# Kernel optimization log

Hardware: AMD Instinct MI355X
Metric: run time of the kernel (lower is better)

The kernel has to match this reference:

```python
import jax, jax.numpy as jnp
import numpy as np

WS = 16          # window_size
OWS = 24         # overlap_win_size = int(ws*0.5) + ws
PAD = (OWS - WS) // 2
NH = 6           # num_heads


def _ln(x, g, b):
    m = jnp.mean(x, axis=-1, keepdims=True)
    v = jnp.mean((x - m) ** 2, axis=-1, keepdims=True)
    return (x - m) * jax.lax.rsqrt(v + 1e-5) * g + b


def setup_inputs() -> dict:
    key = jax.random.key(0)
    ks = jax.random.split(key, 12)
    B, H, W, C = 4, 64, 64, 180
    std = 0.02
    x = jax.random.normal(ks[0], (B, H * W, C), jnp.float32)
    y = jax.random.normal(ks[1], (B, H * W, C), jnp.float32)
    kv_w = jax.random.normal(ks[2], (2 * C, C), jnp.float32) * std
    kv_b = jnp.zeros((2 * C,), jnp.float32)
    q_w = jax.random.normal(ks[3], (C, C), jnp.float32) * std
    q_b = jnp.zeros((C,), jnp.float32)
    rpb = jax.random.normal(ks[4], ((WS + OWS - 1) ** 2, NH), jnp.float32) * std
    proj_w = jax.random.normal(ks[5], (C, C), jnp.float32) * std
    proj_b = jnp.zeros((C,), jnp.float32)
    fc1_w = jax.random.normal(ks[6], (4 * C, C), jnp.float32) * std
    fc1_b = jnp.zeros((4 * C,), jnp.float32)
    fc2_w = jax.random.normal(ks[7], (C, 4 * C), jnp.float32) * std
    fc2_b = jnp.zeros((C,), jnp.float32)
    norm1_g = jnp.ones((C,), jnp.float32); norm1_b = jnp.zeros((C,), jnp.float32)
    norm2_g = jnp.ones((C,), jnp.float32); norm2_b = jnp.zeros((C,), jnp.float32)
    # relative position index (HAT-style OCA): query coords vs extended window coords
    co = np.stack(np.meshgrid(np.arange(WS), np.arange(WS), indexing='ij')).reshape(2, -1)   # 2, ws*ws
    ce = np.stack(np.meshgrid(np.arange(OWS), np.arange(OWS), indexing='ij')).reshape(2, -1) # 2, ows*ows
    rel = (ce[:, None, :] - co[:, :, None]).transpose(1, 2, 0) + (WS - 1)  # nq, n, 2 in [0, ws+ows-2]
    rpi = jnp.asarray(rel[..., 0] * (WS + OWS - 1) + rel[..., 1], jnp.int32)  # [256, 576]
    return {
        'x': x, 'y': y,
        'norm1_g': norm1_g, 'norm1_b': norm1_b,
        'kv_w': kv_w, 'kv_b': kv_b, 'q_w': q_w, 'q_b': q_b,
        'rpb': rpb, 'proj_w': proj_w, 'proj_b': proj_b,
        'norm2_g': norm2_g, 'norm2_b': norm2_b,
        'fc1_w': fc1_w, 'fc1_b': fc1_b, 'fc2_w': fc2_w, 'fc2_b': fc2_b,
        'rpi': rpi, 'h': 64, 'w': 64,
    }


def reference(x, y, norm1_g, norm1_b, kv_w, kv_b, q_w, q_b, rpb, proj_w, proj_b,
              norm2_g, norm2_b, fc1_w, fc1_b, fc2_w, fc2_b, rpi, h, w):
    b, L, c = x.shape
    nh = NH
    d = c // nh
    scale = d ** -0.5
    nwh, nww = h // WS, w // WS
    nq, n = WS * WS, OWS * OWS

    shortcut = x
    xn = _ln(x, norm1_g, norm1_b).reshape(b, h, w, c)
    yn = _ln(y, norm1_g, norm1_b).reshape(b, h, w, c)

    kv = xn @ kv_w.T + kv_b                                  # b,h,w,2c
    q = yn @ q_w.T + q_b                                     # b,h,w,c

    # kv -> [2, b, c, h, w] then pad spatially and extract overlapping windows (nn.Unfold)
    kv = kv.reshape(b, h, w, 2, c).transpose(3, 0, 4, 1, 2)  # 2,b,c,h,w
    kvp = jnp.pad(kv, ((0, 0), (0, 0), (0, 0), (PAD, PAD), (PAD, PAD)))
    hh = jnp.arange(nwh)[:, None] * WS + jnp.arange(OWS)[None, :]   # [nwh, OWS]
    ww = jnp.arange(nww)[:, None] * WS + jnp.arange(OWS)[None, :]   # [nww, OWS]
    patches = kvp[:, :, :, hh][:, :, :, :, :, ww]            # 2,b,c,nwh,OWS,nww,OWS
    kvw = patches.transpose(0, 1, 3, 5, 4, 6, 2).reshape(2, b * nwh * nww, n, c)
    kwin, vwin = kvw[0], kvw[1]                              # [b_, n, c]

    # non-overlapping query windows (window_partition)
    qwin = q.reshape(b, nwh, WS, nww, WS, c).transpose(0, 1, 3, 2, 4, 5).reshape(-1, nq, c)
    b_ = qwin.shape[0]

    qh = qwin.reshape(b_, nq, nh, d).transpose(0, 2, 1, 3) * scale
    kh = kwin.reshape(b_, n, nh, d).transpose(0, 2, 1, 3)
    vh = vwin.reshape(b_, n, nh, d).transpose(0, 2, 1, 3)

    attn = jnp.einsum('bhqd,bhkd->bhqk', qh, kh)             # [b_, nh, nq, n]
    bias = rpb[rpi.reshape(-1)].reshape(nq, n, nh).transpose(2, 0, 1)  # [nh, nq, n]
    attn = jax.nn.softmax(attn + bias[None], axis=-1)
    out = jnp.einsum('bhqk,bhkd->bhqd', attn, vh).transpose(0, 2, 1, 3).reshape(b_, nq, c)

    # window_reverse
    out = out.reshape(b, nwh, nww, WS, WS, c).transpose(0, 1, 3, 2, 4, 5).reshape(b, h * w, c)

    xo = out @ proj_w.T + proj_b + shortcut
    xn2 = _ln(xo, norm2_g, norm2_b)
    mlp = jax.nn.gelu(xn2 @ fc1_w.T + fc1_b, approximate=False) @ fc2_w.T + fc2_b
    return xo + mlp
```

## Files before the change

kernel.cpp:

```cpp
#include <hip/hip_runtime.h>

typedef __bf16 bf16;
typedef __bf16 bf16x8 __attribute__((ext_vector_type(8)));
typedef __bf16 bf16x4 __attribute__((ext_vector_type(4)));
typedef __bf16 bf16x2 __attribute__((ext_vector_type(2)));
typedef float f32x4 __attribute__((ext_vector_type(4)));

static __device__ __forceinline__ bf16x8 ld8(const bf16* p) {
    return *reinterpret_cast<const bf16x8*>(p);
}
static __device__ __forceinline__ bf16x4 ld4(const bf16* p) {
    return *reinterpret_cast<const bf16x4*>(p);
}
static __device__ __forceinline__ bf16x8 ld8_b32(const bf16* p) {
    bf16x8 v;
#pragma unroll
    for (int i = 0; i < 4; ++i) {
        bf16x2 t = *reinterpret_cast<const bf16x2*>(p + i * 2);
        v[i * 2] = t[0]; v[i * 2 + 1] = t[1];
    }
    return v;
}
static __device__ __forceinline__ bf16x8 zero8() {
    bf16x8 v;
#pragma unroll
    for (int i = 0; i < 8; ++i) v[i] = (bf16)0.f;
    return v;
}

#define MFMA16(a, b, c) __builtin_amdgcn_mfma_f32_16x16x32_bf16((a), (b), (c), 0, 0, 0)

template <int ROWS, int BK, int KPAD, int THREADS>
static __device__ __forceinline__ void load_chunk_g(const bf16* __restrict__ g,
                                                    bf16x8* r, int tid) {
    constexpr int TOT = ROWS * BK / 8;
    constexpr int NP = (TOT + THREADS - 1) / THREADS;
#pragma unroll
    for (int p = 0; p < NP; ++p) {
        int idx = p * THREADS + tid;
        if ((TOT % THREADS) == 0 || idx < TOT) {
            int row = idx / (BK / 8), cg = idx % (BK / 8);
            r[p] = ld8(g + (long)row * KPAD + cg * 8);
        }
    }
}
template <int ROWS, int BK, int THREADS>
static __device__ __forceinline__ void store_chunk_l(bf16* __restrict__ lds,
                                                     const bf16x8* r, int tid) {
    constexpr int TOT = ROWS * BK / 8;
    constexpr int NP = (TOT + THREADS - 1) / THREADS;
#pragma unroll
    for (int p = 0; p < NP; ++p) {
        int idx = p * THREADS + tid;
        if ((TOT % THREADS) == 0 || idx < TOT) {
            int row = idx / (BK / 8), cg = idx % (BK / 8);
            *reinterpret_cast<bf16x8*>(lds + row * 200 + cg * 8) = r[p];
        }
    }
}
template <int ROWS, int BK, int KPAD, int THREADS>
static __device__ __forceinline__ void stage_tile(const bf16* __restrict__ g,
                                                  bf16* __restrict__ lds, int tid) {
    constexpr int TOT = ROWS * BK / 8;
    constexpr int NP = (TOT + THREADS - 1) / THREADS;
#pragma unroll
    for (int p = 0; p < NP; ++p) {
        int idx = p * THREADS + tid;
        if ((TOT % THREADS) == 0 || idx < TOT) {
            int row = idx / (BK / 8), cg = idx % (BK / 8);
            bf16x8 v = ld8(g + (long)row * KPAD + cg * 8);
            *reinterpret_cast<bf16x8*>(lds + row * 200 + cg * 8) = v;
        }
    }
}

__global__ __launch_bounds__(256) void fused_pre(
    const float* __restrict__ x, const float* __restrict__ y,
    const float* __restrict__ g, const float* __restrict__ b,
    bf16* __restrict__ dst,
    const float* __restrict__ kv_w, const float* __restrict__ kv_b,
    const float* __restrict__ q_w, const float* __restrict__ q_b,
    const float* __restrict__ proj_w, const float* __restrict__ fc1_w,
    const float* __restrict__ fc2_w, const float* __restrict__ rpb,
    const int* __restrict__ rpi,
    bf16* __restrict__ wkv, bf16* __restrict__ wq, bf16* __restrict__ wproj,
    bf16* __restrict__ wfc1, bf16* __restrict__ wfc2, bf16* __restrict__ biast,
    float* __restrict__ kvbp, float* __restrict__ qbp)
{
    for (int u = blockIdx.x; u < 13635; u += 1704) {
        if (u < 8192) {
            int wave = threadIdx.x >> 6, lane = threadIdx.x & 63;
            int row = u * 4 + wave;
            const float* sp = (row < 16384) ? (x + (long)row * 180)
                                            : (y + (long)(row - 16384) * 180);
            float v0 = sp[lane];
            float v1 = sp[lane + 64];
            float v2 = (lane < 52) ? sp[lane + 128] : 0.f;
            float s = v0 + v1 + v2;
            float sq = v0 * v0 + v1 * v1 + v2 * v2;
#pragma unroll
            for (int m = 32; m >= 1; m >>= 1) {
                s += __shfl_xor(s, m);
                sq += __shfl_xor(sq, m);
            }
            float mean = s * (1.f / 180.f);
            float var = sq * (1.f / 180.f) - mean * mean;
            float rs = rsqrtf(var + 1e-5f);
            bf16* dp = dst + (long)row * 192;
            dp[lane] = (bf16)((v0 - mean) * rs * g[lane] + b[lane]);
            dp[lane + 64] = (bf16)((v1 - mean) * rs * g[lane + 64] + b[lane + 64]);
            float o2 = (lane < 52) ? ((v2 - mean) * rs * g[lane + 128] + b[lane + 128]) : 0.f;
            dp[lane + 128] = (bf16)o2;
            continue;
        }
        int i = (u - 8192) * 256 + threadIdx.x;
        if (i < 73728) {
            int n = i / 192, k = i % 192;
            int kv = n / 192, rem = n % 192, hh = rem >> 5, d = rem & 31;
            float v = (d < 30 && k < 180) ? kv_w[(kv * 180 + hh * 30 + d) * 180 + k] : 0.f;
            wkv[i] = (bf16)v;
        } else if (i < 122880) {
            int j = i - 73728; int n = j / 192, k = j % 192;
            int hh = n >> 5, d = n & 31;
            float v = (n < 192 && d < 30 && k < 180) ? q_w[(hh * 30 + d) * 180 + k] : 0.f;
            wq[j] = (bf16)v;
        } else if (i < 172032) {
            int j = i - 122880; int n = j / 192, k = j % 192;
            int hh = k >> 5, d = k & 31;
            float v = (n < 180 && d < 30) ? proj_w[n * 180 + hh * 30 + d] : 0.f;
            wproj[j] = (bf16)v;
        } else if (i < 319488) {
            int j = i - 172032; int n = j / 192, k = j % 192;
            float v = (n < 720 && k < 180) ? fc1_w[n * 180 + k] : 0.f;
            wfc1[j] = (bf16)v;
        } else if (i < 507904) {
            int j = i - 319488; int n = j / 736, k = j % 736;
            float v = (n < 180 && k < 720) ? fc2_w[n * 720 + k] : 0.f;
            wfc2[j] = (bf16)v;
        } else if (i < 1392640) {
            int t = i - 507904;
            int r = t & 3;
            int lane = (t >> 2) & 63;
            int tmp2 = t >> 8;
            int kg = tmp2 % 36;
            int tmp3 = tmp2 / 36;
            int qg = tmp3 & 15;
            int h = tmp3 >> 4;
            int q = qg * 16 + (lane & 15);
            int key = kg * 16 + ((lane >> 4) << 2) + r;
            biast[t] = (bf16)rpb[rpi[q * 576 + key] * 6 + h];
        } else if (i < 1393024) {
            int t = i - 1392640;
            int kv = t / 192, rem = t % 192, hh = rem >> 5, d = rem & 31;
            kvbp[t] = (d < 30) ? kv_b[kv * 180 + hh * 30 + d] : 0.f;
        } else if (i < 1393216) {
            int t = i - 1393024;
            int hh = t >> 5, d = t & 31;
            qbp[t] = (d < 30) ? q_b[hh * 30 + d] * 0.18257418583505537f : 0.f;
        }
    }
}

__global__ __launch_bounds__(256, 3) void gemm_kvq(
    const bf16* __restrict__ xn, const bf16* __restrict__ yn,
    const bf16* __restrict__ wkv, const bf16* __restrict__ wq,
    const float* __restrict__ kvbp, const float* __restrict__ qbp,
    bf16* __restrict__ kvbuf, bf16* __restrict__ qbuf)
{
    const int tid = threadIdx.x, wave = tid >> 6, lane = tid & 63;
    const int llo = lane & 15, quad = lane >> 4;
    const int phys = blockIdx.x;
    const int xcd = phys & 7, idx = phys >> 3;
    const int tmi = xcd * 32 + idx / 3;
    const int bz = idx % 3;
    const bool isq = (bz == 2);
    const bf16* A = isq ? yn : xn;
    const bf16* Wbase = isq ? wq : (wkv + (long)bz * 3 * 64 * 192);
    const int tm = tmi * 64;

    __shared__ __align__(16) bf16 Sa[64 * 200];
    __shared__ __align__(16) bf16 Sb[64 * 200];
    bf16* Sc = Sb;

    stage_tile<64, 192, 192, 256>(A + (long)tm * 192, Sa, tid);
    bf16x8 wreg[6];
    load_chunk_g<64, 192, 192, 256>(Wbase, wreg, tid);

    const float sc = isq ? 0.18257418583505537f : 1.f;

    for (int s = 0; s < 3; ++s) {
        if (s) __syncthreads();
        store_chunk_l<64, 192, 256>(Sb, wreg, tid);
        __syncthreads();
        if (s < 2) load_chunk_g<64, 192, 192, 256>(Wbase + (long)(s + 1) * 64 * 192, wreg, tid);

        f32x4 acc[4];
#pragma unroll
        for (int nt = 0; nt < 4; ++nt)
#pragma unroll
            for (int r = 0; r < 4; ++r) acc[nt][r] = 0.f;
#pragma unroll
        for (int kt = 0; kt < 6; ++kt) {
            bf16x8 a = ld8(Sa + (wave * 16 + llo) * 200 + kt * 32 + quad * 8);
#pragma unroll
            for (int nt = 0; nt < 4; ++nt) {
                bf16x8 b = ld8(Sb + (nt * 16 + llo) * 200 + kt * 32 + quad * 8);
                acc[nt] = MFMA16(a, b, acc[nt]);
            }
        }

        const int grp = bz * 3 + s;
        __syncthreads();
#pragma unroll
        for (int nt = 0; nt < 4; ++nt) {
            int n = grp * 64 + nt * 16 + llo;
            float bv = isq ? qbp[n - 384] : kvbp[n];
#pragma unroll
            for (int r = 0; r < 4; ++r)
                Sc[(wave * 16 + quad * 4 + r) * 72 + nt * 16 + llo] =
                    (bf16)(acc[nt][r] * sc + bv);
        }
        __syncthreads();
#pragma unroll
        for (int ps = 0; ps < 2; ++ps) {
            int un = ps * 256 + tid;
            int row = un >> 3, seg = un & 7;
            bf16x8 vv = *reinterpret_cast<const bf16x8*>(Sc + row * 72 + seg * 8);
            long m = tm + row;
            if (!isq)
                *reinterpret_cast<bf16x8*>(kvbuf + m * 384 + grp * 64 + seg * 8) = vv;
            else
                *reinterpret_cast<bf16x8*>(qbuf + m * 192 + (grp - 6) * 64 + seg * 8) = vv;
        }
    }
}

__global__ __launch_bounds__(512, 6) void attn_kernel(
    const bf16* __restrict__ qbuf, const bf16* __restrict__ kvbuf,
    const bf16* __restrict__ biast, bf16* __restrict__ obuf)
{
    const int phys = blockIdx.x;
    const int xcd = phys & 7, idx = phys >> 3;
    const int win = xcd * 8 + idx / 12;
    const int sub = idx % 12;
    const int qhalf = sub & 1;
    const int head = sub >> 1;
    const int bb = win / 16, wi = (win % 16) / 4, wj = win % 4;
    const int tid = threadIdx.x;
    const int wave = tid >> 6, lane = tid & 63;
    const int llo = lane & 15, quad = lane >> 4;
    const int qbase = qhalf * 128 + wave * 16;
    const int qg = qhalf * 8 + wave;

    __shared__ bf16 Kc[2][64][40];
    __shared__ bf16 Vt[2][32][74];
    __shared__ bf16 Ps[8][16][72];

    const int u = tid & 255;
    const int tloc = u >> 2, dq = u & 3;
    const bool isV = tid >= 256;
    int aa = tloc / 24, w0 = tloc % 24;

    const int q0 = qbase + llo;
    const int gr_q = bb * 4096 + (wi * 16 + (q0 >> 4)) * 64 + (wj * 16 + (q0 & 15));
    const bf16x8 qf = ld8(qbuf + (long)gr_q * 192 + head * 32 + quad * 8);
    const bf16* bbase = biast + ((long)(head * 16 + qg) * 36) * 256 + lane * 4;

    {
        int gy = wi * 16 + aa - 4, gx = wj * 16 + w0 - 4;
        bf16x8 st = zero8();
        if ((unsigned)gy < 64u && (unsigned)gx < 64u) {
            long gr = (long)(bb * 4096 + gy * 64 + gx) * 384;
            st = ld8(kvbuf + gr + (isV ? 192 : 0) + head * 32 + dq * 8);
        }
        if (!isV) {
            *reinterpret_cast<bf16x8*>(&Kc[0][tloc][dq * 8]) = st;
        } else {
#pragma unroll
            for (int j = 0; j < 8; ++j) Vt[0][dq * 8 + j][tloc] = st[j];
        }
    }
    __syncthreads();

    f32x4 o[2];
    float m_run = -1e30f, l_run = 0.f;
#pragma unroll
    for (int n2 = 0; n2 < 2; ++n2)
#pragma unroll
        for (int r = 0; r < 4; ++r) o[n2][r] = 0.f;

    for (int c = 0; c < 9; ++c) {
        const int cur = c & 1;

        bf16x8 stage;
        if (c < 8) {
            w0 += 16; aa += 2;
            if (w0 >= 24) { w0 -= 24; ++aa; }
            int gy = wi * 16 + aa - 4, gx = wj * 16 + w0 - 4;
            stage = zero8();
            if ((unsigned)gy < 64u && (unsigned)gx < 64u) {
                long gr = (long)(bb * 4096 + gy * 64 + gx) * 384;
                stage = ld8(kvbuf + gr + (isV ? 192 : 0) + head * 32 + dq * 8);
            }
        }

        f32x4 s[4];
#pragma unroll
        for (int kt = 0; kt < 4; ++kt) {
            bf16x8 kf = ld8(&Kc[cur][kt * 16 + llo][quad * 8]);
            f32x4 zc;
            zc[0] = 0.f; zc[1] = 0.f; zc[2] = 0.f; zc[3] = 0.f;
            s[kt] = MFMA16(kf, qf, zc);
        }

#pragma unroll
        for (int kt = 0; kt < 4; ++kt) {
            bf16x4 bv = ld4(bbase + (c * 4 + kt) * 256);
#pragma unroll
            for (int r = 0; r < 4; ++r) s[kt][r] += (float)bv[r];
        }

        float mx = s[0][0];
#pragma unroll
        for (int kt = 0; kt < 4; ++kt)
#pragma unroll
            for (int r = 0; r < 4; ++r) mx = fmaxf(mx, s[kt][r]);
        mx = fmaxf(mx, __shfl_xor(mx, 16));
        mx = fmaxf(mx, __shfl_xor(mx, 32));
        float m_new = fmaxf(m_run, mx);
        float alpha = __expf(m_run - m_new);
        float ls = 0.f;
#pragma unroll
        for (int kt = 0; kt < 4; ++kt)
#pragma unroll
            for (int r = 0; r < 4; ++r) {
                float p = __expf(s[kt][r] - m_new);
                s[kt][r] = p;
                ls += p;
            }
        ls += __shfl_xor(ls, 16);
        ls += __shfl_xor(ls, 32);
        l_run = l_run * alpha + ls;
        m_run = m_new;

#pragma unroll
        for (int r = 0; r < 4; ++r) {
            float a = __shfl(alpha, quad * 4 + r);
            o[0][r] *= a;
            o[1][r] *= a;
        }

#pragma unroll
        for (int kt = 0; kt < 4; ++kt) {
            bf16x4 pv;
#pragma unroll
            for (int r = 0; r < 4; ++r) pv[r] = (bf16)s[kt][r];
            *reinterpret_cast<bf16x4*>(&Ps[wave][llo][kt * 16 + quad * 4]) = pv;
        }

#pragma unroll
        for (int kt2 = 0; kt2 < 2; ++kt2) {
            bf16x8 pa = ld8(&Ps[wave][llo][kt2 * 32 + quad * 8]);
#pragma unroll
            for (int n2 = 0; n2 < 2; ++n2) {
                bf16x8 vb = ld8_b32(&Vt[cur][n2 * 16 + llo][kt2 * 32 + quad * 8]);
                o[n2] = MFMA16(pa, vb, o[n2]);
            }
        }

        if (c < 8) {
            if (!isV) {
                *reinterpret_cast<bf16x8*>(&Kc[1 - cur][tloc][dq * 8]) = stage;
            } else {
#pragma unroll
                for (int j = 0; j < 8; ++j) Vt[1 - cur][dq * 8 + j][tloc] = stage[j];
            }
            __syncthreads();
        }
    }

    float linv = 1.f / l_run;
#pragma unroll
    for (int r = 0; r < 4; ++r) {
        float li = __shfl(linv, quad * 4 + r);
        int q = qbase + quad * 4 + r;
        int gr = bb * 4096 + (wi * 16 + (q >> 4)) * 64 + (wj * 16 + (q & 15));
#pragma unroll
        for (int n2 = 0; n2 < 2; ++n2)
            obuf[(long)gr * 192 + head * 32 + n2 * 16 + llo] = (bf16)(o[n2][r] * li);
    }
}

__global__ __launch_bounds__(256, 3) void gemm_projln(
    const bf16* __restrict__ obuf, const bf16* __restrict__ wproj,
    const float* __restrict__ proj_b, const float* __restrict__ x,
    const float* __restrict__ g, const float* __restrict__ bln,
    float* __restrict__ xo, bf16* __restrict__ xn2)
{
    const int tid = threadIdx.x, wave = tid >> 6, lane = tid & 63;
    const int llo = lane & 15, quad = lane >> 4;
    const int mbase = blockIdx.x * 64;

    __shared__ __align__(16) bf16 Sa[64 * 200];
    __shared__ __align__(16) bf16 Sb[64 * 200];
    stage_tile<64, 192, 192, 256>(obuf + (long)mbase * 192, Sa, tid);
    bf16x8 wreg[6];
    load_chunk_g<64, 192, 192, 256>(wproj, wreg, tid);

    f32x4 acc[12];
#pragma unroll
    for (int nt = 0; nt < 12; ++nt)
#pragma unroll
        for (int r = 0; r < 4; ++r) acc[nt][r] = 0.f;

    for (int nc = 0; nc < 3; ++nc) {
        if (nc) __syncthreads();
        store_chunk_l<64, 192, 256>(Sb, wreg, tid);
        __syncthreads();
        if (nc < 2) load_chunk_g<64, 192, 192, 256>(wproj + (long)(nc + 1) * 64 * 192, wreg, tid);
#pragma unroll
        for (int kt = 0; kt < 6; ++kt) {
            bf16x8 a = ld8(Sa + (wave * 16 + llo) * 200 + kt * 32 + quad * 8);
#pragma unroll
            for (int nt = 0; nt < 4; ++nt) {
                bf16x8 b = ld8(Sb + (nt * 16 + llo) * 200 + kt * 32 + quad * 8);
                acc[nc * 4 + nt] = MFMA16(a, b, acc[nc * 4 + nt]);
            }
        }
    }

#pragma unroll
    for (int r = 0; r < 4; ++r) {
        int m = mbase + wave * 16 + quad * 4 + r;
        float v[12];
        float sum = 0.f, sq = 0.f;
#pragma unroll
        for (int nt = 0; nt < 12; ++nt) {
            int n = nt * 16 + llo;
            float val = 0.f;
            if (n < 180) val = acc[nt][r] + proj_b[n] + x[(long)m * 180 + n];
            v[nt] = val;
            sum += val; sq += val * val;
        }
#pragma unroll
        for (int msk = 1; msk <= 8; msk <<= 1) {
            sum += __shfl_xor(sum, msk);
            sq  += __shfl_xor(sq, msk);
        }
        float mean = sum * (1.f / 180.f);
        float var = sq * (1.f / 180.f) - mean * mean;
        float rs = rsqrtf(var + 1e-5f);
#pragma unroll
        for (int nt = 0; nt < 12; ++nt) {
            int n = nt * 16 + llo;
            if (n < 180) {
                xo[(long)m * 180 + n] = v[nt];
                xn2[(long)m * 192 + n] = (bf16)((v[nt] - mean) * rs * g[n] + bln[n]);
            } else {
                xn2[(long)m * 192 + n] = (bf16)0.f;
            }
        }
    }
}

__global__ __launch_bounds__(512, 4) void gemm_fc1(
    const bf16* __restrict__ A, const bf16* __restrict__ W,
    const float* __restrict__ bias, bf16* __restrict__ outp)
{
    const int tid = threadIdx.x, wave = tid >> 6, lane = tid & 63;
    const int llo = lane & 15, quad = lane >> 4;
    const int phys = blockIdx.x;
    const int xcd = phys & 7, idx = phys >> 3;
    const int tmi = xcd * 16 + idx / 4;
    const int bz = idx % 4;
    const int tm = tmi * 128;
    const bf16* Wbase = W + (long)bz * 3 * 64 * 192;

    __shared__ __align__(16) bf16 Sa[128 * 200];
    __shared__ __align__(16) bf16 Sb[64 * 200];
    bf16* Sc = Sb;

    stage_tile<128, 192, 192, 512>(A + (long)tm * 192, Sa, tid);
    bf16x8 wreg[3];
    load_chunk_g<64, 192, 192, 512>(Wbase, wreg, tid);

    for (int s = 0; s < 3; ++s) {
        if (s) __syncthreads();
        store_chunk_l<64, 192, 512>(Sb, wreg, tid);
        __syncthreads();
        if (s < 2) load_chunk_g<64, 192, 192, 512>(Wbase + (long)(s + 1) * 64 * 192, wreg, tid);

        f32x4 acc[4];
#pragma unroll
        for (int nt = 0; nt < 4; ++nt)
#pragma unroll
            for (int r = 0; r < 4; ++r) acc[nt][r] = 0.f;
#pragma unroll
        for (int kt = 0; kt < 6; ++kt) {
            bf16x8 a = ld8(Sa + (wave * 16 + llo) * 200 + kt * 32 + quad * 8);
#pragma unroll
            for (int nt = 0; nt < 4; ++nt) {
                bf16x8 b = ld8(Sb + (nt * 16 + llo) * 200 + kt * 32 + quad * 8);
                acc[nt] = MFMA16(a, b, acc[nt]);
            }
        }

        const int nb = (bz * 3 + s) * 64;
        __syncthreads();
#pragma unroll
        for (int nt = 0; nt < 4; ++nt) {
            int n = nb + nt * 16 + llo;
            float bv = (n < 720) ? bias[n] : 0.f;
#pragma unroll
            for (int r = 0; r < 4; ++r) {
                float v = acc[nt][r] + bv;
                float gel = 0.5f * v * (1.f + erff(v * 0.7071067811865475f));
                Sc[(wave * 16 + quad * 4 + r) * 72 + nt * 16 + llo] = (bf16)gel;
            }
        }
        __syncthreads();
        const int row8 = tid >> 3, seg = tid & 7;
        if (nb + seg * 8 < 736) {
#pragma unroll
            for (int ps = 0; ps < 2; ++ps) {
                int row = ps * 64 + row8;
                bf16x8 vv = *reinterpret_cast<const bf16x8*>(Sc + row * 72 + seg * 8);
                *reinterpret_cast<bf16x8*>(outp + (long)(tm + row) * 736 + nb + seg * 8) = vv;
            }
        }
    }
}

__global__ __launch_bounds__(256, 4) void gemm_fc2(
    const bf16* __restrict__ A, const bf16* __restrict__ W,
    const float* __restrict__ bias, const float* __restrict__ resid,
    float* __restrict__ outp)
{
    const int tid = threadIdx.x, wave = tid >> 6, lane = tid & 63;
    const int llo = lane & 15, quad = lane >> 4;
    const int phys = blockIdx.x;
    const int xcd = phys & 7, idx = phys >> 3;
    const int tmi = xcd * 32 + idx / 3;
    const int tni = idx % 3;
    const int tm = tmi * 64;
    const int tn = tni * 64;

    __shared__ __align__(16) bf16 Sa[64 * 200];
    __shared__ __align__(16) bf16 Sb[64 * 200];

    const bf16* Ap = A + (long)tm * 736;
    const bf16* Wp = W + (long)tn * 736;

    bf16x8 ar[6], wr[6];
    load_chunk_g<64, 192, 736, 256>(Ap, ar, tid);
    load_chunk_g<64, 192, 736, 256>(Wp, wr, tid);

    f32x4 acc[4];
#pragma unroll
    for (int nt = 0; nt < 4; ++nt)
#pragma unroll
        for (int r = 0; r < 4; ++r) acc[nt][r] = 0.f;

#pragma unroll
    for (int c = 0; c < 4; ++c) {
        if (c) __syncthreads();
        if (c < 3) {
            store_chunk_l<64, 192, 256>(Sa, ar, tid);
            store_chunk_l<64, 192, 256>(Sb, wr, tid);
        } else {
            store_chunk_l<64, 160, 256>(Sa, ar, tid);
            store_chunk_l<64, 160, 256>(Sb, wr, tid);
        }
        __syncthreads();
        if (c < 2) {
            load_chunk_g<64, 192, 736, 256>(Ap + (c + 1) * 192, ar, tid);
            load_chunk_g<64, 192, 736, 256>(Wp + (c + 1) * 192, wr, tid);
        } else if (c == 2) {
            load_chunk_g<64, 160, 736, 256>(Ap + 576, ar, tid);
            load_chunk_g<64, 160, 736, 256>(Wp + 576, wr, tid);
        }
        const int nkt = (c == 3) ? 5 : 6;
        for (int kt = 0; kt < nkt; ++kt) {
            bf16x8 a = ld8(Sa + (wave * 16 + llo) * 200 + kt * 32 + quad * 8);
#pragma unroll
            for (int nt = 0; nt < 4; ++nt) {
                bf16x8 b = ld8(Sb + (nt * 16 + llo) * 200 + kt * 32 + quad * 8);
                acc[nt] = MFMA16(a, b, acc[nt]);
            }
        }
    }

#pragma unroll
    for (int nt = 0; nt < 4; ++nt)
#pragma unroll
        for (int r = 0; r < 4; ++r) {
            int m = tm + wave * 16 + quad * 4 + r;
            int n = tn + nt * 16 + llo;
            if (n >= 180) continue;
            float v = acc[nt][r] + bias[n];
            outp[(long)m * 180 + n] = v + resid[(long)m * 180 + n];
        }
}

extern "C" void kernel_launch(void* const* d_in, const int* in_sizes, int n_in,
                              void* d_out, int out_size, void* d_ws, size_t ws_size,
                              hipStream_t stream) {
    const float* x      = (const float*)d_in[0];
    const float* y      = (const float*)d_in[1];
    const float* n1g    = (const float*)d_in[2];
    const float* n1b    = (const float*)d_in[3];
    const float* kv_w   = (const float*)d_in[4];
    const float* kv_b   = (const float*)d_in[5];
    const float* q_w    = (const float*)d_in[6];
    const float* q_b    = (const float*)d_in[7];
    const float* rpb    = (const float*)d_in[8];
    const float* proj_w = (const float*)d_in[9];
    const float* proj_b = (const float*)d_in[10];
    const float* n2g    = (const float*)d_in[11];
    const float* n2b    = (const float*)d_in[12];
    const float* fc1_w  = (const float*)d_in[13];
    const float* fc1_b  = (const float*)d_in[14];
    const float* fc2_w  = (const float*)d_in[15];
    const float* fc2_b  = (const float*)d_in[16];
    const int*   rpi    = (const int*)d_in[17];

    char* ws = (char*)d_ws;
    bf16* xn    = (bf16*)(ws + 0);
    bf16* yn    = (bf16*)(ws + 6291456);
    bf16* qbuf  = (bf16*)(ws + 12582912);
    bf16* kvbuf = (bf16*)(ws + 18874368);
    bf16* obuf  = (bf16*)(ws + 31457280);
    float* xo   = (float*)(ws + 37748736);
    bf16* biast = (bf16*)(ws + 49545216);
    bf16* wkv   = (bf16*)(ws + 51314688);
    bf16* wq    = (bf16*)(ws + 51462144);
    bf16* wproj = (bf16*)(ws + 51560448);
    bf16* wfc1  = (bf16*)(ws + 51658752);
    bf16* wfc2  = (bf16*)(ws + 51953664);
    float* kvbp = (float*)(ws + 52428800);
    float* qbp  = (float*)(ws + 52430336);
    bf16* hmid  = (bf16*)(ws + 6291456);
    bf16* xn2   = xn;

    fused_pre<<<1704, 256, 0, stream>>>(x, y, n1g, n1b, xn,
                                        kv_w, kv_b, q_w, q_b,
                                        proj_w, fc1_w, fc2_w, rpb, rpi,
                                        wkv, wq, wproj, wfc1, wfc2, biast,
                                        kvbp, qbp);
    gemm_kvq<<<768, 256, 0, stream>>>(xn, yn, wkv, wq, kvbp, qbp, kvbuf, qbuf);
    attn_kernel<<<768, 512, 0, stream>>>(qbuf, kvbuf, biast, obuf);
    gemm_projln<<<256, 256, 0, stream>>>(obuf, wproj, proj_b, x, n2g, n2b, xo, xn2);
    gemm_fc1<<<512, 512, 0, stream>>>(xn2, wfc1, fc1_b, hmid);
    gemm_fc2<<<768, 256, 0, stream>>>(hmid, wfc2, fc2_b, xo, (float*)d_out);
}
```

Before: 195.0 us.

## Fuse fc1 and fc2 MLP GEMMs into one kernel keeping hidden tile in LDS

New measurement: 198.9 us. About the same (+2.0%).

```diff
diff --git a/kernel.cpp b/kernel.cpp
--- a/kernel.cpp
+++ b/kernel.cpp
@@ -463,143 +463,110 @@
     }
 }
 
-__global__ __launch_bounds__(512, 4) void gemm_fc1(
-    const bf16* __restrict__ A, const bf16* __restrict__ W,
-    const float* __restrict__ bias, bf16* __restrict__ outp)
-{
-    const int tid = threadIdx.x, wave = tid >> 6, lane = tid & 63;
-    const int llo = lane & 15, quad = lane >> 4;
-    const int phys = blockIdx.x;
-    const int xcd = phys & 7, idx = phys >> 3;
-    const int tmi = xcd * 16 + idx / 4;
-    const int bz = idx % 4;
-    const int tm = tmi * 128;
-    const bf16* Wbase = W + (long)bz * 3 * 64 * 192;
-
-    __shared__ __align__(16) bf16 Sa[128 * 200];
-    __shared__ __align__(16) bf16 Sb[64 * 200];
-    bf16* Sc = Sb;
-
-    stage_tile<128, 192, 192, 512>(A + (long)tm * 192, Sa, tid);
-    bf16x8 wreg[3];
-    load_chunk_g<64, 192, 192, 512>(Wbase, wreg, tid);
-
-    for (int s = 0; s < 3; ++s) {
-        if (s) __syncthreads();
-        store_chunk_l<64, 192, 512>(Sb, wreg, tid);
-        __syncthreads();
-        if (s < 2) load_chunk_g<64, 192, 192, 512>(Wbase + (long)(s + 1) * 64 * 192, wreg, tid);
-
-        f32x4 acc[4];
-#pragma unroll
-        for (int nt = 0; nt < 4; ++nt)
-#pragma unroll
-            for (int r = 0; r < 4; ++r) acc[nt][r] = 0.f;
-#pragma unroll
-        for (int kt = 0; kt < 6; ++kt) {
-            bf16x8 a = ld8(Sa + (wave * 16 + llo) * 200 + kt * 32 + quad * 8);
-#pragma unroll
-            for (int nt = 0; nt < 4; ++nt) {
-                bf16x8 b = ld8(Sb + (nt * 16 + llo) * 200 + kt * 32 + quad * 8);
-                acc[nt] = MFMA16(a, b, acc[nt]);
-            }
-        }
-
-        const int nb = (bz * 3 + s) * 64;
-        __syncthreads();
-#pragma unroll
-        for (int nt = 0; nt < 4; ++nt) {
-            int n = nb + nt * 16 + llo;
-            float bv = (n < 720) ? bias[n] : 0.f;
-#pragma unroll
-            for (int r = 0; r < 4; ++r) {
-                float v = acc[nt][r] + bv;
-                float gel = 0.5f * v * (1.f + erff(v * 0.7071067811865475f));
-                Sc[(wave * 16 + quad * 4 + r) * 72 + nt * 16 + llo] = (bf16)gel;
-            }
-        }
-        __syncthreads();
-        const int row8 = tid >> 3, seg = tid & 7;
-        if (nb + seg * 8 < 736) {
-#pragma unroll
-            for (int ps = 0; ps < 2; ++ps) {
-                int row = ps * 64 + row8;
-                bf16x8 vv = *reinterpret_cast<const bf16x8*>(Sc + row * 72 + seg * 8);
-                *reinterpret_cast<bf16x8*>(outp + (long)(tm + row) * 736 + nb + seg * 8) = vv;
-            }
-        }
-    }
-}
-
-__global__ __launch_bounds__(256, 4) void gemm_fc2(
-    const bf16* __restrict__ A, const bf16* __restrict__ W,
-    const float* __restrict__ bias, const float* __restrict__ resid,
+__global__ __launch_bounds__(256, 2) void gemm_mlp(
+    const bf16* __restrict__ A, const bf16* __restrict__ W1,
+    const float* __restrict__ b1, const bf16* __restrict__ W2,
+    const float* __restrict__ b2, const float* __restrict__ resid,
     float* __restrict__ outp)
 {
     const int tid = threadIdx.x, wave = tid >> 6, lane = tid & 63;
     const int llo = lane & 15, quad = lane >> 4;
     const int phys = blockIdx.x;
     const int xcd = phys & 7, idx = phys >> 3;
-    const int tmi = xcd * 32 + idx / 3;
-    const int tni = idx % 3;
-    const int tm = tmi * 64;
-    const int tn = tni * 64;
-
-    __shared__ __align__(16) bf16 Sa[64 * 200];
+    const int tmi = xcd * 64 + idx;
+    const int tm = tmi * 32;
+    const int wr = wave & 1, wn = wave >> 1;
+
+    __shared__ __align__(16) bf16 Hm[32][744];
     __shared__ __align__(16) bf16 Sb[64 * 200];
 
-    const bf16* Ap = A + (long)tm * 736;
-    const bf16* Wp = W + (long)tn * 736;
-
-    bf16x8 ar[6], wr[6];
-    load_chunk_g<64, 192, 736, 256>(Ap, ar, tid);
-    load_chunk_g<64, 192, 736, 256>(Wp, wr, tid);
-
-    f32x4 acc[4];
-#pragma unroll
-    for (int nt = 0; nt < 4; ++nt)
-#pragma unroll
-        for (int r = 0; r < 4; ++r) acc[nt][r] = 0.f;
-
-#pragma unroll
-    for (int c = 0; c < 4; ++c) {
-        if (c) __syncthreads();
-        if (c < 3) {
-            store_chunk_l<64, 192, 256>(Sa, ar, tid);
-            store_chunk_l<64, 192, 256>(Sb, wr, tid);
-        } else {
-            store_chunk_l<64, 160, 256>(Sa, ar, tid);
-            store_chunk_l<64, 160, 256>(Sb, wr, tid);
-        }
+    bf16x8 af[6];
+    {
+        const bf16* ap = A + (long)(tm + wr * 16 + llo) * 192 + quad * 8;
+#pragma unroll
+        for (int kt = 0; kt < 6; ++kt) af[kt] = ld8(ap + kt * 32);
+    }
+
+    bf16x8 wreg[6];
+    load_chunk_g<64, 192, 192, 256>(W1, wreg, tid);
+
+    for (int ch = 0; ch < 12; ++ch) {
+        if (ch) __syncthreads();
+        store_chunk_l<64, 192, 256>(Sb, wreg, tid);
         __syncthreads();
-        if (c < 2) {
-            load_chunk_g<64, 192, 736, 256>(Ap + (c + 1) * 192, ar, tid);
-            load_chunk_g<64, 192, 736, 256>(Wp + (c + 1) * 192, wr, tid);
-        } else if (c == 2) {
-            load_chunk_g<64, 160, 736, 256>(Ap + 576, ar, tid);
-            load_chunk_g<64, 160, 736, 256>(Wp + 576, wr, tid);
-        }
-        const int nkt = (c == 3) ? 5 : 6;
-        for (int kt = 0; kt < nkt; ++kt) {
-            bf16x8 a = ld8(Sa + (wave * 16 + llo) * 200 + kt * 32 + quad * 8);
-#pragma unroll
-            for (int nt = 0; nt < 4; ++nt) {
-                bf16x8 b = ld8(Sb + (nt * 16 + llo) * 200 + kt * 32 + quad * 8);
-                acc[nt] = MFMA16(a, b, acc[nt]);
-            }
-        }
-    }
-
-#pragma unroll
-    for (int nt = 0; nt < 4; ++nt)
-#pragma unroll
-        for (int r = 0; r < 4; ++r) {
-            int m = tm + wave * 16 + quad * 4 + r;
-            int n = tn + nt * 16 + llo;
-            if (n >= 180) continue;
-            float v = acc[nt][r] + bias[n];
-            outp[(long)m * 180 + n] = v + resid[(long)m * 180 + n];
-        }
+        if (ch < 11) load_chunk_g<64, 192, 192, 256>(W1 + (long)(ch + 1) * 64 * 192, wreg, tid);
+        else         load_chunk_g<64, 192, 736, 256>(W2, wreg, tid);
+
+        f32x4 acc[2];
+#pragma unroll
+        for (int nt = 0; nt < 2; ++nt)
+#pragma unroll
+            for (int r = 0; r < 4; ++r) acc[nt][r] = 0.f;
+#pragma unroll
+        for (int kt = 0; kt < 6; ++kt) {
+#pragma unroll
+            for (int nt = 0; nt < 2; ++nt) {
+                bf16x8 b = ld8(Sb + ((wn * 2 + nt) * 16 + llo) * 200 + kt * 32 + quad * 8);
+                acc[nt] = MFMA16(af[kt], b, acc[nt]);
+            }
+        }
+        const int nb = ch * 64;
+#pragma unroll
+        for (int nt = 0; nt < 2; ++nt) {
+            int n = nb + (wn * 2 + nt) * 16 + llo;
+            if (n < 736) {
+                float bv = (n < 720) ? b1[n] : 0.f;
+#pragma unroll
+                for (int r = 0; r < 4; ++r) {
+                    float v = acc[nt][r] + bv;
+                    float gel = 0.5f * v * (1.f + erff(v * 0.7071067811865475f));
+                    Hm[wr * 16 + quad * 4 + r][n] = (bf16)gel;
+                }
+            }
+        }
+    }
+
+    for (int nc = 0; nc < 3; ++nc) {
+        f32x4 acc2[2];
+#pragma unroll
+        for (int nt = 0; nt < 2; ++nt)
+#pragma unroll
+            for (int r = 0; r < 4; ++r) acc2[nt][r] = 0.f;
+        for (int kc = 0; kc < 4; ++kc) {
+            __syncthreads();
+            if (kc < 3) store_chunk_l<64, 192, 256>(Sb, wreg, tid);
+            else        store_chunk_l<64, 160, 256>(Sb, wreg, tid);
+            __syncthreads();
+            const int cc = nc * 4 + kc;
+            if (cc < 11) {
+                int nc2 = (cc + 1) >> 2, kc2 = (cc + 1) & 3;
+                const bf16* p = W2 + (long)nc2 * 64 * 736 + kc2 * 192;
+                if (kc2 == 3) load_chunk_g<64, 160, 736, 256>(p, wreg, tid);
+                else          load_chunk_g<64, 192, 736, 256>(p, wreg, tid);
+            }
+            const int nkt = (kc == 3) ? 5 : 6;
+            for (int kt = 0; kt < nkt; ++kt) {
+                bf16x8 a = ld8(&Hm[wr * 16 + llo][kc * 192 + kt * 32 + quad * 8]);
+#pragma unroll
+                for (int nt = 0; nt < 2; ++nt) {
+                    bf16x8 b = ld8(Sb + ((wn * 2 + nt) * 16 + llo) * 200 + kt * 32 + quad * 8);
+                    acc2[nt] = MFMA16(a, b, acc2[nt]);
+                }
+            }
+        }
+#pragma unroll
+        for (int nt = 0; nt < 2; ++nt) {
+            int n = nc * 64 + (wn * 2 + nt) * 16 + llo;
+            if (n < 180) {
+                float bv = b2[n];
+#pragma unroll
+                for (int r = 0; r < 4; ++r) {
+                    int m = tm + wr * 16 + quad * 4 + r;
+                    outp[(long)m * 180 + n] = acc2[nt][r] + bv + resid[(long)m * 180 + n];
+                }
+            }
+        }
+    }
 }
 
 extern "C" void kernel_launch(void* const* d_in, const int* in_sizes, int n_in,
@@ -639,7 +606,6 @@
     bf16* wfc2  = (bf16*)(ws + 51953664);
     float* kvbp = (float*)(ws + 52428800);
     float* qbp  = (float*)(ws + 52430336);
-    bf16* hmid  = (bf16*)(ws + 6291456);
     bf16* xn2   = xn;
 
     fused_pre<<<1704, 256, 0, stream>>>(x, y, n1g, n1b, xn,
@@ -650,6 +616,5 @@
     gemm_kvq<<<768, 256, 0, stream>>>(xn, yn, wkv, wq, kvbp, qbp, kvbuf, qbuf);
     attn_kernel<<<768, 512, 0, stream>>>(qbuf, kvbuf, biast, obuf);
     gemm_projln<<<256, 256, 0, stream>>>(obuf, wproj, proj_b, x, n2g, n2b, xo, xn2);
-    gemm_fc1<<<512, 512, 0, stream>>>(xn2, wfc1, fc1_b, hmid);
-    gemm_fc2<<<768, 256, 0, stream>>>(hmid, wfc2, fc2_b, xo, (float*)d_out);
-}
+    gemm_mlp<<<512, 256, 0, stream>>>(xn2, wfc1, fc1_b, wfc2, fc2_b, xo, (float*)d_out);
+}
```

## Fuse norm1 LayerNorm into KV/Q GEMM prologue instead of precompute kernel

Applied to the files above, without the earlier changes.

After: 201.7 us. 1.03x slower.

```diff
diff --git a/kernel.cpp b/kernel.cpp
--- a/kernel.cpp
+++ b/kernel.cpp
@@ -75,9 +75,6 @@
 }
 
 __global__ __launch_bounds__(256) void fused_pre(
-    const float* __restrict__ x, const float* __restrict__ y,
-    const float* __restrict__ g, const float* __restrict__ b,
-    bf16* __restrict__ dst,
     const float* __restrict__ kv_w, const float* __restrict__ kv_b,
     const float* __restrict__ q_w, const float* __restrict__ q_b,
     const float* __restrict__ proj_w, const float* __restrict__ fc1_w,
@@ -87,33 +84,8 @@
     bf16* __restrict__ wfc1, bf16* __restrict__ wfc2, bf16* __restrict__ biast,
     float* __restrict__ kvbp, float* __restrict__ qbp)
 {
-    for (int u = blockIdx.x; u < 13635; u += 1704) {
-        if (u < 8192) {
-            int wave = threadIdx.x >> 6, lane = threadIdx.x & 63;
-            int row = u * 4 + wave;
-            const float* sp = (row < 16384) ? (x + (long)row * 180)
-                                            : (y + (long)(row - 16384) * 180);
-            float v0 = sp[lane];
-            float v1 = sp[lane + 64];
-            float v2 = (lane < 52) ? sp[lane + 128] : 0.f;
-            float s = v0 + v1 + v2;
-            float sq = v0 * v0 + v1 * v1 + v2 * v2;
-#pragma unroll
-            for (int m = 32; m >= 1; m >>= 1) {
-                s += __shfl_xor(s, m);
-                sq += __shfl_xor(sq, m);
-            }
-            float mean = s * (1.f / 180.f);
-            float var = sq * (1.f / 180.f) - mean * mean;
-            float rs = rsqrtf(var + 1e-5f);
-            bf16* dp = dst + (long)row * 192;
-            dp[lane] = (bf16)((v0 - mean) * rs * g[lane] + b[lane]);
-            dp[lane + 64] = (bf16)((v1 - mean) * rs * g[lane + 64] + b[lane + 64]);
-            float o2 = (lane < 52) ? ((v2 - mean) * rs * g[lane + 128] + b[lane + 128]) : 0.f;
-            dp[lane + 128] = (bf16)o2;
-            continue;
-        }
-        int i = (u - 8192) * 256 + threadIdx.x;
+    for (int u = blockIdx.x; u < 5443; u += 1704) {
+        int i = u * 256 + threadIdx.x;
         if (i < 73728) {
             int n = i / 192, k = i % 192;
             int kv = n / 192, rem = n % 192, hh = rem >> 5, d = rem & 31;
@@ -162,7 +134,8 @@
 }
 
 __global__ __launch_bounds__(256, 3) void gemm_kvq(
-    const bf16* __restrict__ xn, const bf16* __restrict__ yn,
+    const float* __restrict__ x, const float* __restrict__ y,
+    const float* __restrict__ n1g, const float* __restrict__ n1b,
     const bf16* __restrict__ wkv, const bf16* __restrict__ wq,
     const float* __restrict__ kvbp, const float* __restrict__ qbp,
     bf16* __restrict__ kvbuf, bf16* __restrict__ qbuf)
@@ -174,7 +147,7 @@
     const int tmi = xcd * 32 + idx / 3;
     const int bz = idx % 3;
     const bool isq = (bz == 2);
-    const bf16* A = isq ? yn : xn;
+    const float* src = isq ? y : x;
     const bf16* Wbase = isq ? wq : (wkv + (long)bz * 3 * 64 * 192);
     const int tm = tmi * 64;
 
@@ -182,9 +155,32 @@
     __shared__ __align__(16) bf16 Sb[64 * 200];
     bf16* Sc = Sb;
 
-    stage_tile<64, 192, 192, 256>(A + (long)tm * 192, Sa, tid);
     bf16x8 wreg[6];
     load_chunk_g<64, 192, 192, 256>(Wbase, wreg, tid);
+
+#pragma unroll 2
+    for (int it = 0; it < 16; ++it) {
+        int rl = wave * 16 + it;
+        const float* sp = src + (long)(tm + rl) * 180;
+        float v0 = sp[lane];
+        float v1 = sp[lane + 64];
+        float v2 = (lane < 52) ? sp[lane + 128] : 0.f;
+        float s = v0 + v1 + v2;
+        float sq = v0 * v0 + v1 * v1 + v2 * v2;
+#pragma unroll
+        for (int m = 32; m >= 1; m >>= 1) {
+            s += __shfl_xor(s, m);
+            sq += __shfl_xor(sq, m);
+        }
+        float mean = s * (1.f / 180.f);
+        float var = sq * (1.f / 180.f) - mean * mean;
+        float rs = rsqrtf(var + 1e-5f);
+        bf16* dp = Sa + rl * 200;
+        dp[lane] = (bf16)((v0 - mean) * rs * n1g[lane] + n1b[lane]);
+        dp[lane + 64] = (bf16)((v1 - mean) * rs * n1g[lane + 64] + n1b[lane + 64]);
+        float o2 = (lane < 52) ? ((v2 - mean) * rs * n1g[lane + 128] + n1b[lane + 128]) : 0.f;
+        dp[lane + 128] = (bf16)o2;
+    }
 
     const float sc = isq ? 0.18257418583505537f : 1.f;
 
@@ -626,7 +622,6 @@
 
     char* ws = (char*)d_ws;
     bf16* xn    = (bf16*)(ws + 0);
-    bf16* yn    = (bf16*)(ws + 6291456);
     bf16* qbuf  = (bf16*)(ws + 12582912);
     bf16* kvbuf = (bf16*)(ws + 18874368);
     bf16* obuf  = (bf16*)(ws + 31457280);
@@ -642,12 +637,11 @@
     bf16* hmid  = (bf16*)(ws + 6291456);
     bf16* xn2   = xn;
 
-    fused_pre<<<1704, 256, 0, stream>>>(x, y, n1g, n1b, xn,
-                                        kv_w, kv_b, q_w, q_b,
+    fused_pre<<<1704, 256, 0, stream>>>(kv_w, kv_b, q_w, q_b,
                                         proj_w, fc1_w, fc2_w, rpb, rpi,
                                         wkv, wq, wproj, wfc1, wfc2, biast,
                                         kvbp, qbp);
-    gemm_kvq<<<768, 256, 0, stream>>>(xn, yn, wkv, wq, kvbp, qbp, kvbuf, qbuf);
+    gemm_kvq<<<768, 256, 0, stream>>>(x, y, n1g, n1b, wkv, wq, kvbp, qbp, kvbuf, qbuf);
     attn_kernel<<<768, 512, 0, stream>>>(qbuf, kvbuf, biast, obuf);
     gemm_projln<<<256, 256, 0, stream>>>(obuf, wproj, proj_b, x, n2g, n2b, xo, xn2);
     gemm_fc1<<<512, 512, 0, stream>>>(xn2, wfc1, fc1_b, hmid);
```
